# Kernel optimization log

Hardware: AMD Instinct MI355X
Metric: run time of the kernel (lower is better)

The kernel has to match this reference:

```python
import jax, jax.numpy as jnp
import numpy as np

B, N, E, D, F_IN, EDGE_DIM, VN = 128, 500, 1048576, 128, 5, 2, 10
NEG_FEAT = 0.01   # torch F.leaky_relu default
NEG_ATT = 0.2     # GAT attention slope


def _gat_layer(h_in, src, dst, edge_attr, W, b, a_src, a_dst, a_edge, We, n_nodes):
    # Edge-feature GAT conv: per-edge attention over (src, dst, edge) then
    # softmax-normalized scatter-aggregate onto destination nodes.
    h = h_in @ W                                  # [N, d]
    e = edge_attr @ We                            # [E, d] projected edge features
    logits = jax.nn.leaky_relu((h @ a_src)[src] + (h @ a_dst)[dst] + e @ a_edge,
                               negative_slope=NEG_ATT)    # [E]
    # segment softmax over incoming edges of each dst node
    m = jax.ops.segment_max(logits, dst, num_segments=n_nodes)
    ex = jnp.exp(logits - m[dst])
    denom = jax.ops.segment_sum(ex, dst, num_segments=n_nodes)
    alpha = ex / (denom[dst] + 1e-16)             # [E]
    msg = h[src] + e                              # [E, d]
    out = jax.ops.segment_sum(alpha[:, None] * msg, dst, num_segments=n_nodes)
    return out + b


def setup_inputs() -> dict:
    key = jax.random.key(0)
    ks = jax.random.split(key, 20)
    s = 0.05
    return {
        'x': jax.random.normal(ks[0], (B * N, F_IN), jnp.float32),
        'edge_index': jax.random.randint(ks[1], (2, E), 0, B * N, jnp.int64 if jax.config.jax_enable_x64 else jnp.int32).astype(jnp.int32),
        'edge_attr': jax.random.uniform(ks[2], (E, EDGE_DIM), jnp.float32),
        'curr_v_node_id': jax.random.randint(ks[3], (B,), 0, VN).astype(jnp.int32),
        'v_graph_embedding': jax.random.normal(ks[4], (B, D), jnp.float32),
        'v_node_dense_embeddings': jax.random.normal(ks[5], (B, VN, D), jnp.float32),
        'p_W': jax.random.normal(ks[6], (F_IN, D), jnp.float32) * s,
        'p_b': jnp.zeros((D,), jnp.float32),
        'Ws': jax.random.normal(ks[7], (4, D, D), jnp.float32) * s,
        'bs': jnp.zeros((4, D), jnp.float32),
        'a_srcs': jax.random.normal(ks[8], (4, D), jnp.float32) * s,
        'a_dsts': jax.random.normal(ks[9], (4, D), jnp.float32) * s,
        'a_edges': jax.random.normal(ks[10], (4, D), jnp.float32) * s,
        'Wes': jax.random.normal(ks[11], (4, EDGE_DIM, D), jnp.float32) * s,
        'W5': jax.random.normal(ks[12], (D, 1), jnp.float32) * s,
        'b5': jnp.zeros((1,), jnp.float32),
        'a_src5': jax.random.normal(ks[13], (1,), jnp.float32) * s,
        'a_dst5': jax.random.normal(ks[14], (1,), jnp.float32) * s,
        'a_edge5': jax.random.normal(ks[15], (1,), jnp.float32) * s,
        'We5': jax.random.normal(ks[16], (EDGE_DIM, 1), jnp.float32) * s,
    }


def reference(x, edge_index, edge_attr, curr_v_node_id, v_graph_embedding,
              v_node_dense_embeddings, p_W, p_b, Ws, bs, a_srcs, a_dsts,
              a_edges, Wes, W5, b5, a_src5, a_dst5, a_edge5, We5):
    n_nodes = x.shape[0]
    src, dst = edge_index[0], edge_index[1]
    # gather current v-node embedding: [B, D]
    curr_emb = v_node_dense_embeddings[jnp.arange(B), curr_v_node_id]
    # linear + leaky_relu then broadcast-add of graph/node context
    h = jax.nn.leaky_relu(x @ p_W + p_b, negative_slope=NEG_FEAT)  # [B*N, D]
    h = h.reshape(B, N, D) + v_graph_embedding[:, None, :] + curr_emb[:, None, :]
    h = h.reshape(B * N, D)
    # 4 hidden edge-feature GAT layers (128 -> 128) with leaky_relu
    for l in range(4):
        h = _gat_layer(h, src, dst, edge_attr, Ws[l], bs[l], a_srcs[l],
                       a_dsts[l], a_edges[l], Wes[l], n_nodes)
        h = jax.nn.leaky_relu(h, negative_slope=NEG_FEAT)
    # output layer (128 -> 1), no activation
    h = _gat_layer(h, src, dst, edge_attr, W5, b5, a_src5, a_dst5, a_edge5,
                   We5, n_nodes)                    # [B*N, 1]
    return h.reshape(B, N)
```

## Files before the change

### kernel.cpp

```cpp
#include <hip/hip_runtime.h>
#include <hip/hip_bf16.h>

#define BB   128
#define NN   500
#define NV   64000
#define EE   1048576
#define DD   128
#define FIN  5
#define VNN  10
#define NBUK 250
#define BCAP 8192

typedef unsigned int   uint32;
typedef unsigned short u16b;
typedef __attribute__((ext_vector_type(8))) short short8;
typedef __attribute__((ext_vector_type(4))) float float4v;
typedef __attribute__((ext_vector_type(2))) float float2v;

#define P_ASRC  0
#define P_ADST  512
#define P_WE    1024
#define P_BIAS  2048
#define P_W5    2560
#define P_CVEC  2688
#define P_SC5   2700
#define P_ASD   2816
#define P_TOT   3840

static __device__ __forceinline__ float bf2f(__hip_bfloat16 v) { return __bfloat162float(v); }
static __device__ __forceinline__ float lo2f(uint32 u) { return __uint_as_float(u << 16); }
static __device__ __forceinline__ float hi2f(uint32 u) { return __uint_as_float(u & 0xFFFF0000u); }
static __device__ __forceinline__ uint32 f2bf_bits(float f) {
    uint32 u = __float_as_uint(f);
    return (u + 0x7FFFu + ((u >> 16) & 1u)) >> 16;
}
static __device__ __forceinline__ uint32 pack2(float a, float b) {
    return (f2bf_bits(a) & 0xFFFFu) | (f2bf_bits(b) << 16);
}
static __device__ __forceinline__ float2v unp2(uint32 u) {
    float2v r; r.x = lo2f(u); r.y = hi2f(u); return r;
}
static __device__ __forceinline__ float2v fma2(float2v a, float2v b, float2v c) {
#if __has_builtin(__builtin_elementwise_fma)
    return __builtin_elementwise_fma(a, b, c);
#else
    float2v r; r.x = fmaf(a.x, b.x, c.x); r.y = fmaf(a.y, b.y, c.y); return r;
#endif
}
static __device__ __forceinline__ float2v fma2s(float2v a, float w, float2v c) {
    float2v ww = {w, w};
    return fma2(a, ww, c);
}
static __device__ __forceinline__ float2v shfl_xor2(float2v v, int o) {
    double d; __builtin_memcpy(&d, &v, 8);
    d = __shfl_xor(d, o, 64);
    float2v r; __builtin_memcpy(&r, &d, 8);
    return r;
}
static __device__ __forceinline__ float2v lrelu2(float2v x, float slope) {
    float2v z = {0.f, 0.f};
#if __has_builtin(__builtin_elementwise_max)
    float2v p = __builtin_elementwise_max(x, z);
    float2v q = __builtin_elementwise_min(x, z);
#else
    float2v p; p.x = fmaxf(x.x, 0.f); p.y = fmaxf(x.y, 0.f);
    float2v q; q.x = fminf(x.x, 0.f); q.y = fminf(x.y, 0.f);
#endif
    float2v s = {slope, slope};
    return fma2(q, s, p);
}
static __device__ __forceinline__ float ldf(const void* p, int i, int flag) {
    return flag ? ((const float*)p)[i] : bf2f(((const __hip_bfloat16*)p)[i]);
}

__global__ void sniff_init_kernel(const unsigned short* __restrict__ p16,
                                  int* __restrict__ FLAG, int* __restrict__ gcur,
                                  int* __restrict__ counts) {
    if (blockIdx.x == 0) {
        __shared__ int sHigh, sZero;
        if (threadIdx.x == 0) { sHigh = 0; sZero = 0; }
        __syncthreads();
        unsigned short v = p16[2 * threadIdx.x];
        if (v >= 0x8000u) atomicOr(&sHigh, 1);
        if (v == 0)       atomicAdd(&sZero, 1);
        __syncthreads();
        if (threadIdx.x == 0) FLAG[0] = (sHigh || sZero >= 128) ? 1 : 0;
    } else {
        int t = (blockIdx.x - 1) * 256 + threadIdx.x;
        if (t < NBUK) gcur[t] = t * BCAP;
        if (t < 512) counts[NV + t] = 0;
    }
}

__global__ void zero_out_kernel(void* __restrict__ out, const int* __restrict__ FLAG, float tag) {
    int i = blockIdx.x * blockDim.x + threadIdx.x;
    if (i >= NV) return;
    float v = (i == 0) ? tag : 0.f;
    if (FLAG[0]) ((float*)out)[i] = v;
    else         ((u16b*)out)[i] = (u16b)f2bf_bits(v);
}

__global__ __launch_bounds__(256) void prep_kernel(
        const void* __restrict__ Wes, const void* __restrict__ aeg,
        const void* __restrict__ We5, const void* __restrict__ ae5,
        const void* __restrict__ asr, const void* __restrict__ ads,
        const void* __restrict__ bs, const void* __restrict__ W5,
        const void* __restrict__ b5, const void* __restrict__ as5,
        const void* __restrict__ ad5, const void* __restrict__ Ws,
        const int* __restrict__ FLAG, float* __restrict__ PAR,
        u16b* __restrict__ WB) {
    const int flag = FLAG[0];
    if (blockIdx.x == 0) {
        for (int i = threadIdx.x; i < 512; i += 256) PAR[P_ASRC + i] = ldf(asr, i, flag);
    } else if (blockIdx.x == 1) {
        for (int i = threadIdx.x; i < 512; i += 256) PAR[P_ADST + i] = ldf(ads, i, flag);
    } else if (blockIdx.x == 2) {
        for (int i = threadIdx.x; i < 1024; i += 256) PAR[P_WE + i] = ldf(Wes, i, flag);
    } else if (blockIdx.x == 3) {
        for (int i = threadIdx.x; i < 512; i += 256) PAR[P_BIAS + i] = ldf(bs, i, flag);
    } else if (blockIdx.x == 4) {
        int tid = threadIdx.x;
        if (tid < 128) {
            PAR[P_W5 + tid] = ldf(W5, tid, flag);
        } else if (tid < 136) {
            int l = (tid - 128) >> 1, r = (tid - 128) & 1;
            float s = 0.f;
            for (int ch = 0; ch < DD; ++ch)
                s += ldf(Wes, l * 256 + r * DD + ch, flag) * ldf(aeg, l * DD + ch, flag);
            PAR[P_CVEC + l * 2 + r] = s;
        } else if (tid == 136) {
            float ae = ldf(ae5, 0, flag);
            float w0 = ldf(We5, 0, flag), w1 = ldf(We5, 1, flag);
            PAR[P_CVEC + 8] = w0 * ae; PAR[P_CVEC + 9] = w1 * ae;
            PAR[P_CVEC + 10] = w0;     PAR[P_CVEC + 11] = w1;
            PAR[P_SC5 + 0] = ldf(b5, 0, flag);
            PAR[P_SC5 + 1] = ldf(as5, 0, flag);
            PAR[P_SC5 + 2] = ldf(ad5, 0, flag);
        }
    } else if (blockIdx.x == 5) {
        for (int i = threadIdx.x; i < 512; i += 256) {
            int l = i >> 7, c = i & 127;
            PAR[P_ASD + l * 256 + c * 2]     = ldf(asr, l * DD + c, flag);
            PAR[P_ASD + l * 256 + c * 2 + 1] = ldf(ads, l * DD + c, flag);
        }
    } else {
        int t = (blockIdx.x - 6) * 256 + threadIdx.x;
        int lane = t & 63;
        int frag = t >> 6;
        int nchunk = frag & 7, kblk = (frag >> 3) & 3, l = frag >> 5;
        int n = nchunk * 16 + (lane & 15);
        int kbase = kblk * 32 + (lane >> 4) * 8;
#pragma unroll
        for (int j = 0; j < 8; ++j) {
            int idx = l * 16384 + (kbase + j) * 128 + n;
            u16b bits = flag ? (u16b)f2bf_bits(((const float*)Ws)[idx])
                             : ((const u16b*)Ws)[idx];
            WB[(size_t)t * 8 + j] = bits;
        }
    }
}

__global__ __launch_bounds__(256) void bucketize_kernel(
        const int* __restrict__ src, const int* __restrict__ dst,
        const void* __restrict__ eaP, const int* __restrict__ FLAG,
        int* __restrict__ gcur, uint32* __restrict__ bukx, uint32* __restrict__ buky) {
    __shared__ int cnt[256];
    __shared__ int cur[256];
    const int flag = FLAG[0];
    const int t = threadIdx.x;
    const int e0 = blockIdx.x * 4096;
    cnt[t] = 0;
    __syncthreads();
    int d[16];
#pragma unroll
    for (int i = 0; i < 16; ++i) {
        d[i] = dst[e0 + i * 256 + t];
        if ((unsigned)d[i] >= NV) d[i] = -1;
        if (d[i] >= 0) atomicAdd(&cnt[d[i] >> 8], 1);
    }
    __syncthreads();
    if (t < NBUK) {
        int c = cnt[t];
        cur[t] = c ? atomicAdd(&gcur[t], c) : 0;
    }
    __syncthreads();
#pragma unroll
    for (int i = 0; i < 16; ++i) {
        if (d[i] < 0) continue;
        int e = e0 + i * 256 + t;
        int b = d[i] >> 8;
        int s = src[e];
        if ((unsigned)s >= NV) s = 0;
        uint32 eb;
        if (flag) { float2 v = ((const float2*)eaP)[e]; eb = pack2(v.x, v.y); }
        else      eb = ((const uint32*)eaP)[e];
        int p = atomicAdd(&cur[b], 1);
        if (p < (b + 1) * BCAP) {
            bukx[p] = (uint32)((s & 0xFFFF) | ((d[i] & 255) << 16));
            buky[p] = eb;
        }
    }
}

__global__ __launch_bounds__(256) void bcount_kernel(
        const uint32* __restrict__ bukx, const int* __restrict__ gcur,
        int* __restrict__ counts) {
    __shared__ int c[256];
    const int b = blockIdx.x, t = threadIdx.x;
    c[t] = 0;
    __syncthreads();
    const int base = b * BCAP;
    int cnt = gcur[b] - base;
    if (cnt > BCAP) cnt = BCAP;
    for (int i = t; i < cnt; i += 256)
        atomicAdd(&c[(bukx[base + i] >> 16) & 255], 1);
    __syncthreads();
    counts[b * 256 + t] = c[t];
}

__global__ __launch_bounds__(256) void scan1_kernel(const int* __restrict__ counts,
                                                    int* __restrict__ row_ptr,
                                                    int* __restrict__ partials) {
    __shared__ int sdata[256];
    int tid = threadIdx.x;
    int4 v = ((const int4*)counts)[blockIdx.x * 256 + tid];
    int sum = v.x + v.y + v.z + v.w;
    sdata[tid] = sum;
    __syncthreads();
    int acc = sum;
    for (int off = 1; off < 256; off <<= 1) {
        int t = (tid >= off) ? sdata[tid - off] : 0;
        __syncthreads();
        acc += t;
        sdata[tid] = acc;
        __syncthreads();
    }
    int excl = acc - sum;
    int base = blockIdx.x * 1024 + tid * 4;
    int run = excl;
    if (base + 0 <= NV) row_ptr[base + 0] = run; run += v.x;
    if (base + 1 <= NV) row_ptr[base + 1] = run; run += v.y;
    if (base + 2 <= NV) row_ptr[base + 2] = run; run += v.z;
    if (base + 3 <= NV) row_ptr[base + 3] = run;
    if (tid == 255) partials[blockIdx.x] = acc;
}

__global__ __launch_bounds__(64) void scan2_kernel(const int* __restrict__ partials,
                                                   int* __restrict__ boff, int nb) {
    int lane = threadIdx.x;
    int v = (lane < nb) ? partials[lane] : 0;
    int orig = v;
#pragma unroll
    for (int off = 1; off < 64; off <<= 1) {
        int t = __shfl_up(v, off, 64);
        if (lane >= off) v += t;
    }
    boff[lane] = v - orig;
}

__global__ __launch_bounds__(256) void scan3_kernel(int* __restrict__ row_ptr,
                                                    const int* __restrict__ boff) {
    int add = boff[blockIdx.x];
    int base = blockIdx.x * 1024 + threadIdx.x * 4;
#pragma unroll
    for (int j = 0; j < 4; ++j) {
        int i = base + j;
        if (i <= NV) row_ptr[i] += add;
    }
}

__global__ __launch_bounds__(256) void bscatter_kernel(
        const uint32* __restrict__ bukx, const uint32* __restrict__ buky,
        const int* __restrict__ gcur, const int* __restrict__ row_ptr,
        uint2* __restrict__ csr2) {
    __shared__ int cur[256];
    const int b = blockIdx.x, t = threadIdx.x;
    cur[t] = row_ptr[b * 256 + t];
    __syncthreads();
    const int base = b * BCAP;
    int cnt = gcur[b] - base;
    if (cnt > BCAP) cnt = BCAP;
    for (int i = t; i < cnt; i += 256) {
        uint32 x = bukx[base + i];
        uint32 y = buky[base + i];
        int p = atomicAdd(&cur[(x >> 16) & 255], 1);
        csr2[p] = make_uint2(x & 0xFFFFu, y);
    }
}

__global__ __launch_bounds__(256) void gemm_kernel(
        const uint32* __restrict__ Hu, const u16b* __restrict__ WBl,
        const float* __restrict__ ASDl, uint32* __restrict__ HWu,
        float* __restrict__ ssrc, float* __restrict__ sdst) {
    __shared__ float hs[64 * 129];
    const int tid = threadIdx.x;
    const int lane = tid & 63;
    const int wave = tid >> 6;
    const int quad = lane >> 4;
    const int n0 = blockIdx.x * 64;
    const int m = n0 + wave * 16 + (lane & 15);

    const u16b* hrow = (const u16b*)Hu + (size_t)m * 128;
    short8 a0 = *(const short8*)(hrow + 0  + quad * 8);
    short8 a1 = *(const short8*)(hrow + 32 + quad * 8);
    short8 a2 = *(const short8*)(hrow + 64 + quad * 8);
    short8 a3 = *(const short8*)(hrow + 96 + quad * 8);

    const float2v* asd = (const float2v*)ASDl;
    float2v psd[4];
#pragma unroll
    for (int r = 0; r < 4; ++r) { psd[r].x = 0.f; psd[r].y = 0.f; }

#pragma unroll
    for (int nt = 0; nt < 8; ++nt) {
        const u16b* bbase = WBl + ((size_t)nt * 512 + lane * 8);
        short8 b0 = *(const short8*)(bbase + 0 * 4096);
        short8 b1 = *(const short8*)(bbase + 1 * 4096);
        short8 b2 = *(const short8*)(bbase + 2 * 4096);
        short8 b3 = *(const short8*)(bbase + 3 * 4096);
        float4v acc = {0.f, 0.f, 0.f, 0.f};
        acc = __builtin_amdgcn_mfma_f32_16x16x32_bf16(a0, b0, acc, 0, 0, 0);
        acc = __builtin_amdgcn_mfma_f32_16x16x32_bf16(a1, b1, acc, 0, 0, 0);
        acc = __builtin_amdgcn_mfma_f32_16x16x32_bf16(a2, b2, acc, 0, 0, 0);
        acc = __builtin_amdgcn_mfma_f32_16x16x32_bf16(a3, b3, acc, 0, 0, 0);
        float2v av = asd[nt * 16 + (lane & 15)];
#pragma unroll
        for (int r = 0; r < 4; ++r) {
            hs[(wave * 16 + quad * 4 + r) * 129 + nt * 16 + (lane & 15)] = acc[r];
            psd[r] = fma2s(av, acc[r], psd[r]);
        }
    }
#pragma unroll
    for (int r = 0; r < 4; ++r) {
#pragma unroll
        for (int o = 1; o < 16; o <<= 1) {
            float2v other = shfl_xor2(psd[r], o);
            psd[r].x += other.x; psd[r].y += other.y;
        }
    }
    if ((lane & 15) == 0) {
#pragma unroll
        for (int r = 0; r < 4; ++r) {
            int row = n0 + wave * 16 + quad * 4 + r;
            ssrc[row] = psd[r].x;
            sdst[row] = psd[r].y;
        }
    }
    __syncthreads();

#pragma unroll
    for (int i = 0; i < 4; ++i) {
        int flat = i * 2048 + tid * 8;
        int n = flat >> 7, c = flat & 127;
        const float* p = hs + n * 129 + c;
        uint4 v;
        v.x = pack2(p[0], p[1]); v.y = pack2(p[2], p[3]);
        v.z = pack2(p[4], p[5]); v.w = pack2(p[6], p[7]);
        *(uint4*)(HWu + (size_t)(n0 + n) * 64 + c / 2) = v;
    }
}

__global__ __launch_bounds__(256) void gemm_proj_kernel(
        const void* __restrict__ x, const void* __restrict__ pW,
        const void* __restrict__ pb, const int* __restrict__ curr,
        const void* __restrict__ vge, const void* __restrict__ vnd,
        const int* __restrict__ FLAG,
        const u16b* __restrict__ WBl, const float* __restrict__ ASDl,
        uint32* __restrict__ HWu, float* __restrict__ ssrc,
        float* __restrict__ sdst) {
    __shared__ float hs[64 * 129];
    uint32* Hl = (uint32*)hs;
    const int flag = FLAG[0];
    const int tid = threadIdx.x;
    const int lane = tid & 63;
    const int wave = tid >> 6;
    const int quad = lane >> 4;
    const int n0 = blockIdx.x * 64;

    {
        const int r = tid & 63;
        const int half = tid >> 6;
        const int n = n0 + r;
        const int b = n / NN;
        int cv = curr[b]; if ((unsigned)cv >= VNN) cv = 0;
        float xv[FIN];
#pragma unroll
        for (int k = 0; k < FIN; ++k) xv[k] = ldf(x, n * FIN + k, flag);
#pragma unroll
        for (int p = 0; p < 16; ++p) {
            const int c = half * 32 + p * 2;
            float s0 = ldf(pb, c, flag), s1 = ldf(pb, c + 1, flag);
#pragma unroll
            for (int k = 0; k < FIN; ++k) {
                s0 = fmaf(xv[k], ldf(pW, k * DD + c, flag), s0);
                s1 = fmaf(xv[k], ldf(pW, k * DD + c + 1, flag), s1);
            }
            s0 = (s0 > 0.f) ? s0 : 0.01f * s0;
            s1 = (s1 > 0.f) ? s1 : 0.01f * s1;
            s0 += ldf(vge, b * DD + c, flag) + ldf(vnd, (b * VNN + cv) * DD + c, flag);
            s1 += ldf(vge, b * DD + c + 1, flag) + ldf(vnd, (b * VNN + cv) * DD + c + 1, flag);
            Hl[r * 68 + half * 16 + p] = pack2(s0, s1);
        }
    }
    __syncthreads();

    const int mloc = wave * 16 + (lane & 15);
    short8 a0 = *(const short8*)(Hl + mloc * 68 + 0 * 16 + quad * 4);
    short8 a1 = *(const short8*)(Hl + mloc * 68 + 1 * 16 + quad * 4);
    short8 a2 = *(const short8*)(Hl + mloc * 68 + 2 * 16 + quad * 4);
    short8 a3 = *(const short8*)(Hl + mloc * 68 + 3 * 16 + quad * 4);
    __syncthreads();

    const float2v* asd = (const float2v*)ASDl;
    float2v psd[4];
#pragma unroll
    for (int r = 0; r < 4; ++r) { psd[r].x = 0.f; psd[r].y = 0.f; }

#pragma unroll
    for (int nt = 0; nt < 8; ++nt) {
        const u16b* bbase = WBl + ((size_t)nt * 512 + lane * 8);
        short8 b0 = *(const short8*)(bbase + 0 * 4096);
        short8 b1 = *(const short8*)(bbase + 1 * 4096);
        short8 b2 = *(const short8*)(bbase + 2 * 4096);
        short8 b3 = *(const short8*)(bbase + 3 * 4096);
        float4v acc = {0.f, 0.f, 0.f, 0.f};
        acc = __builtin_amdgcn_mfma_f32_16x16x32_bf16(a0, b0, acc, 0, 0, 0);
        acc = __builtin_amdgcn_mfma_f32_16x16x32_bf16(a1, b1, acc, 0, 0, 0);
        acc = __builtin_amdgcn_mfma_f32_16x16x32_bf16(a2, b2, acc, 0, 0, 0);
        acc = __builtin_amdgcn_mfma_f32_16x16x32_bf16(a3, b3, acc, 0, 0, 0);
        float2v av = asd[nt * 16 + (lane & 15)];
#pragma unroll
        for (int r = 0; r < 4; ++r) {
            hs[(wave * 16 + quad * 4 + r) * 129 + nt * 16 + (lane & 15)] = acc[r];
            psd[r] = fma2s(av, acc[r], psd[r]);
        }
    }
#pragma unroll
    for (int r = 0; r < 4; ++r) {
#pragma unroll
        for (int o = 1; o < 16; o <<= 1) {
            float2v other = shfl_xor2(psd[r], o);
            psd[r].x += other.x; psd[r].y += other.y;
        }
    }
    if ((lane & 15) == 0) {
#pragma unroll
        for (int r = 0; r < 4; ++r) {
            int row = n0 + wave * 16 + quad * 4 + r;
            ssrc[row] = psd[r].x;
            sdst[row] = psd[r].y;
        }
    }
    __syncthreads();

#pragma unroll
    for (int i = 0; i < 4; ++i) {
        int flat = i * 2048 + tid * 8;
        int n = flat >> 7, c = flat & 127;
        const float* p = hs + n * 129 + c;
        uint4 v;
        v.x = pack2(p[0], p[1]); v.y = pack2(p[2], p[3]);
        v.z = pack2(p[4], p[5]); v.w = pack2(p[6], p[7]);
        *(uint4*)(HWu + (size_t)(n0 + n) * 64 + c / 2) = v;
    }
}

__global__ __launch_bounds__(256) void agg_kernel(
        const uint32* __restrict__ HWu, const float* __restrict__ ssrc,
        const float* __restrict__ sdst, const uint2* __restrict__ csr2,
        const int* __restrict__ row_ptr, const float* __restrict__ PAR,
        int layer, uint32* __restrict__ HoutU,
        float* __restrict__ hw5out, int wantw5) {
    __shared__ float exs[4][64];
    const int lane = threadIdx.x & 63;
    const int wid = threadIdx.x >> 6;
    const int n = blockIdx.x * 4 + wid;
    const int begin = __builtin_amdgcn_readfirstlane(row_ptr[n]);
    const int deg   = __builtin_amdgcn_readfirstlane(row_ptr[n + 1]) - begin;
    const float c0 = PAR[P_CVEC + 2 * layer], c1 = PAR[P_CVEC + 2 * layer + 1];
    const float sd = sdst[n];

    int   sv = 0;
    uint32 eb = 0;
    if (lane < deg) {
        uint2 se = csr2[begin + lane];
        sv = (int)se.x;
        eb = se.y;
    }
    const float ssv = ssrc[sv];

    const int dmain = (deg < 64) ? deg : 64;
    const int npad  = (dmain + 15) & ~15;

    uint32 hA[16], hB[16];
#pragma unroll
    for (int q = 0; q < 16; ++q) {
        int s = __builtin_amdgcn_readlane(sv, q);
        hA[q] = HWu[(s << 6) + lane];
    }
    if (npad > 16) {
#pragma unroll
        for (int q = 0; q < 16; ++q) {
            int s = __builtin_amdgcn_readlane(sv, 16 + q);
            hB[q] = HWu[(s << 6) + lane];
        }
    }

    float ex = 0.f;
    if (lane < deg) {
        float L = fmaf(hi2f(eb), c1, fmaf(lo2f(eb), c0, ssv + sd));
        L = (L > 0.f) ? L : 0.2f * L;
        ex = __expf(fminf(L, 60.f));
    }
    exs[wid][lane] = ex;

    float2v acc2 = {0.f, 0.f};
    const float* wp = &exs[wid][0];
#pragma unroll
    for (int q0 = 0; q0 < 16; q0 += 4) {
        float4 w4 = *(const float4*)(wp + q0);
        acc2 = fma2s(unp2(hA[q0 + 0]), w4.x, acc2);
        acc2 = fma2s(unp2(hA[q0 + 1]), w4.y, acc2);
        acc2 = fma2s(unp2(hA[q0 + 2]), w4.z, acc2);
        acc2 = fma2s(unp2(hA[q0 + 3]), w4.w, acc2);
    }
    if (npad > 16) {
#pragma unroll
        for (int q0 = 16; q0 < 32; q0 += 4) {
            float4 w4 = *(const float4*)(wp + q0);
            acc2 = fma2s(unp2(hB[q0 - 16]), w4.x, acc2);
            acc2 = fma2s(unp2(hB[q0 - 15]), w4.y, acc2);
            acc2 = fma2s(unp2(hB[q0 - 14]), w4.z, acc2);
            acc2 = fma2s(unp2(hB[q0 - 13]), w4.w, acc2);
        }
    }
    for (int j = 32; j < dmain; ++j) {
        int s = __builtin_amdgcn_readlane(sv, j);
        float w = wp[j];
        acc2 = fma2s(unp2(HWu[(s << 6) + lane]), w, acc2);
    }

    float dsum = ex;
    float2v sxy = unp2(eb);
    sxy.x *= ex; sxy.y *= ex;
    for (int j0 = 64; j0 < deg; j0 += 64) {
        int j = j0 + lane;
        if (j < deg) {
            uint2 se2 = csr2[begin + j];
            float L2 = fmaf(hi2f(se2.y), c1, fmaf(lo2f(se2.y), c0, ssrc[se2.x] + sd));
            L2 = (L2 > 0.f) ? L2 : 0.2f * L2;
            float x2 = __expf(fminf(L2, 60.f));
            dsum += x2;
            sxy = fma2s(unp2(se2.y), x2, sxy);
        }
    }
#pragma unroll
    for (int o = 32; o; o >>= 1) {
        dsum += __shfl_xor(dsum, o, 64);
        float2v other = shfl_xor2(sxy, o);
        sxy.x += other.x; sxy.y += other.y;
    }

    for (int jj = 64; jj < deg; ++jj) {
        uint2 se2 = csr2[begin + jj];
        float L2 = fmaf(hi2f(se2.y), c1, fmaf(lo2f(se2.y), c0, ssrc[se2.x] + sd));
        L2 = (L2 > 0.f) ? L2 : 0.2f * L2;
        float x2 = __expf(fminf(L2, 60.f));
        acc2 = fma2s(unp2(HWu[(size_t)se2.x * 64 + lane]), x2, acc2);
    }

    const int ch = lane * 2;
    const float* WEl = PAR + P_WE + layer * 256;
    const float inv = __builtin_amdgcn_rcpf(dsum + 1e-16f);
    const float* Bl = PAR + P_BIAS + layer * DD;
    float2v we0 = *(const float2v*)(WEl + ch);
    float2v we1 = *(const float2v*)(WEl + DD + ch);
    float2v bl  = *(const float2v*)(Bl + ch);
    float2v t2 = fma2s(we1, sxy.y, fma2s(we0, sxy.x, acc2));
    float2v o2 = fma2s(t2, inv, bl);
    o2 = lrelu2(o2, 0.01f);

    if (!wantw5) {
        HoutU[(size_t)n * 64 + lane] = pack2(o2.x, o2.y);
    } else {
        float p = o2.x * PAR[P_W5 + ch] + o2.y * PAR[P_W5 + ch + 1];
#pragma unroll
        for (int o = 32; o; o >>= 1) p += __shfl_xor(p, o, 64);
        if (lane == 0) hw5out[n] = p;
    }
}

__global__ __launch_bounds__(256) void final_kernel(
        const float* __restrict__ hw5, const uint2* __restrict__ csr2,
        const int* __restrict__ row_ptr, const float* __restrict__ PAR,
        const int* __restrict__ FLAG, void* __restrict__ out) {
    const int flag = FLAG[0];
    int lane = threadIdx.x & 63;
    int n = blockIdx.x * 4 + (threadIdx.x >> 6);
    int begin = __builtin_amdgcn_readfirstlane(row_ptr[n]);
    int deg   = __builtin_amdgcn_readfirstlane(row_ptr[n + 1]) - begin;
    float c50 = PAR[P_CVEC + 8], c51 = PAR[P_CVEC + 9];
    float ce0 = PAR[P_CVEC + 10], ce1 = PAR[P_CVEC + 11];
    float b5v = PAR[P_SC5], a5s = PAR[P_SC5 + 1];
    float hd = PAR[P_SC5 + 2] * hw5[n];

    float dsum = 0.f, msum = 0.f;
    for (int j0 = 0; j0 < deg; j0 += 64) {
        int j = j0 + lane;
        if (j < deg) {
            uint2 se = csr2[begin + j];
            float hs5 = hw5[se.x];
            float L = fmaf(hi2f(se.y), c51, fmaf(lo2f(se.y), c50, fmaf(a5s, hs5, hd)));
            L = (L > 0.f) ? L : 0.2f * L;
            float ex = __expf(fminf(L, 60.f));
            dsum += ex;
            msum = fmaf(ex, hs5 + fmaf(hi2f(se.y), ce1, lo2f(se.y) * ce0), msum);
        }
    }
#pragma unroll
    for (int o = 32; o; o >>= 1) {
        dsum += __shfl_xor(dsum, o, 64);
        msum += __shfl_xor(msum, o, 64);
    }
    if (lane == 0) {
        float r = msum * __builtin_amdgcn_rcpf(dsum + 1e-16f) + b5v;
        if (flag) ((float*)out)[n] = r;
        else      ((u16b*)out)[n] = (u16b)f2bf_bits(r);
    }
}

extern "C" void kernel_launch(void* const* d_in, const int* in_sizes, int n_in,
                              void* d_out, int out_size, void* d_ws, size_t ws_size,
                              hipStream_t stream) {
    const void* x   = d_in[0];
    const int*  ei  = (const int*)d_in[1];
    const void* ea  = d_in[2];
    const int*  cur = (const int*)d_in[3];
    const void* vge = d_in[4];
    const void* vnd = d_in[5];
    const void* pW  = d_in[6];
    const void* pb  = d_in[7];
    const void* Ws  = d_in[8];
    const void* bs  = d_in[9];
    const void* asr = d_in[10];
    const void* ads = d_in[11];
    const void* aeg = d_in[12];
    const void* Wes = d_in[13];
    const void* W5  = d_in[14];
    const void* b5  = d_in[15];
    const void* as5 = d_in[16];
    const void* ad5 = d_in[17];
    const void* ae5 = d_in[18];
    const void* We5 = d_in[19];
    (void)in_sizes; (void)n_in; (void)out_size;

    const int* e_src = ei;
    const int* e_dst = ei + EE;

    size_t off = 0;
    char* base = (char*)d_ws;
    auto carve = [&](size_t bytes) {
        void* p = base + off;
        off += (bytes + 255) & ~(size_t)255;
        return p;
    };
    int*    FLAG   = (int*)carve(256);
    float*  PAR    = (float*)carve((size_t)P_TOT * 4);
    u16b*   WB     = (u16b*)carve(4 * DD * DD * 2);
    uint32* H0     = (uint32*)carve((size_t)NV * DD * 2);
    uint32* H1     = (uint32*)carve((size_t)NV * DD * 2);
    float*  SS     = (float*)carve(NV * 4);
    float*  SD     = (float*)carve(NV * 4);
    float*  HW5v   = (float*)carve(NV * 4);
    int*    COUNTS = (int*)carve(65536 * 4);
    int*    ROWPTR = (int*)carve(65536 * 4);
    int*    GCUR   = (int*)carve(256 * 4);
    int*    PART   = (int*)carve(256 * 4);
    int*    BOFF   = (int*)carve(256 * 4);
    uint2*  CSR2   = (uint2*)carve((size_t)EE * 8);
    size_t need = off;

    uint32* BUKX = H1;
    uint32* BUKY = H1 + (size_t)NBUK * BCAP;

    sniff_init_kernel<<<3, 256, 0, stream>>>((const unsigned short*)ea, FLAG,
                                             GCUR, COUNTS);

    if (need > ws_size) {
        zero_out_kernel<<<(NV + 255) / 256, 256, 0, stream>>>(
            d_out, FLAG, (float)(ws_size >> 20));
        return;
    }

    prep_kernel<<<38, 256, 0, stream>>>(Wes, aeg, We5, ae5, asr, ads, bs,
                                        W5, b5, as5, ad5, Ws, FLAG, PAR, WB);

    bucketize_kernel<<<EE / 4096, 256, 0, stream>>>(e_src, e_dst, ea, FLAG,
                                                    GCUR, BUKX, BUKY);
    bcount_kernel<<<NBUK, 256, 0, stream>>>(BUKX, GCUR, COUNTS);
    scan1_kernel<<<63, 256, 0, stream>>>(COUNTS, ROWPTR, PART);
    scan2_kernel<<<1, 64, 0, stream>>>(PART, BOFF, 63);
    scan3_kernel<<<63, 256, 0, stream>>>(ROWPTR, BOFF);
    bscatter_kernel<<<NBUK, 256, 0, stream>>>(BUKX, BUKY, GCUR, ROWPTR, CSR2);

    gemm_proj_kernel<<<NV / 64, 256, 0, stream>>>(
        x, pW, pb, cur, vge, vnd, FLAG, WB, PAR + P_ASD, H1, SS, SD);
    agg_kernel<<<NV / 4, 256, 0, stream>>>(
        H1, SS, SD, CSR2, ROWPTR, PAR, 0, H0, HW5v, 0);
    for (int l = 1; l < 4; ++l) {
        gemm_kernel<<<NV / 64, 256, 0, stream>>>(
            H0, WB + (size_t)l * 16384, PAR + P_ASD + l * 256, H1, SS, SD);
        agg_kernel<<<NV / 4, 256, 0, stream>>>(
            H1, SS, SD, CSR2, ROWPTR, PAR, l, H0, HW5v, (l == 3) ? 1 : 0);
    }

    final_kernel<<<NV / 4, 256, 0, stream>>>(HW5v, CSR2, ROWPTR, PAR,
                                             FLAG, d_out);
}
```

Before: 385.5 us.

## Fuse prep with bucketize, count degrees via global atomics, pack GEMM epilogue in bf16

Merges the weight-prep and edge-bucketize kernels into one launch and removes the separate bucket-count pass by incrementing global per-node counters with atomics during bucketization. A small init kernel zeroes those counters. The GEMM epilogues now pack bf16 pairs via lane shuffles into a smaller shared tile instead of staging full fp32 rows. The aggregation kernel loads neighbor rows in chunks of 8 gated by degree, to avoid wasted gathers for low-degree nodes. The trade-off is about a million global atomics on the counters in exchange for one fewer kernel and pass over the buckets.

```diff
diff --git a/kernel.cpp b/kernel.cpp
--- a/kernel.cpp
+++ b/kernel.cpp
@@ -73,23 +73,15 @@
     return flag ? ((const float*)p)[i] : bf2f(((const __hip_bfloat16*)p)[i]);
 }
 
-__global__ void sniff_init_kernel(const unsigned short* __restrict__ p16,
-                                  int* __restrict__ FLAG, int* __restrict__ gcur,
-                                  int* __restrict__ counts) {
-    if (blockIdx.x == 0) {
-        __shared__ int sHigh, sZero;
-        if (threadIdx.x == 0) { sHigh = 0; sZero = 0; }
-        __syncthreads();
-        unsigned short v = p16[2 * threadIdx.x];
-        if (v >= 0x8000u) atomicOr(&sHigh, 1);
-        if (v == 0)       atomicAdd(&sZero, 1);
-        __syncthreads();
-        if (threadIdx.x == 0) FLAG[0] = (sHigh || sZero >= 128) ? 1 : 0;
-    } else {
-        int t = (blockIdx.x - 1) * 256 + threadIdx.x;
-        if (t < NBUK) gcur[t] = t * BCAP;
-        if (t < 512) counts[NV + t] = 0;
-    }
+__global__ void sniff_kernel(const unsigned short* __restrict__ p16, int* __restrict__ FLAG) {
+    __shared__ int sHigh, sZero;
+    if (threadIdx.x == 0) { sHigh = 0; sZero = 0; }
+    __syncthreads();
+    unsigned short v = p16[2 * threadIdx.x];
+    if (v >= 0x8000u) atomicOr(&sHigh, 1);
+    if (v == 0)       atomicAdd(&sZero, 1);
+    __syncthreads();
+    if (threadIdx.x == 0) FLAG[0] = (sHigh || sZero >= 128) ? 1 : 0;
 }
 
 __global__ void zero_out_kernel(void* __restrict__ out, const int* __restrict__ FLAG, float tag) {
@@ -100,15 +92,25 @@
     else         ((u16b*)out)[i] = (u16b)f2bf_bits(v);
 }
 
-__global__ __launch_bounds__(256) void prep_kernel(
+__global__ void init_kernel(int* __restrict__ gcur, int* __restrict__ counts) {
+    int i = blockIdx.x * 1024 + threadIdx.x * 4;
+    if (i < NV + 512) *(int4*)(counts + i) = make_int4(0, 0, 0, 0);
+    int t = blockIdx.x * 256 + threadIdx.x;
+    if (t < NBUK) gcur[t] = t * BCAP;
+}
+
+__global__ __launch_bounds__(256) void prep_bucketize_kernel(
         const void* __restrict__ Wes, const void* __restrict__ aeg,
         const void* __restrict__ We5, const void* __restrict__ ae5,
         const void* __restrict__ asr, const void* __restrict__ ads,
         const void* __restrict__ bs, const void* __restrict__ W5,
         const void* __restrict__ b5, const void* __restrict__ as5,
         const void* __restrict__ ad5, const void* __restrict__ Ws,
-        const int* __restrict__ FLAG, float* __restrict__ PAR,
-        u16b* __restrict__ WB) {
+        const int* __restrict__ src, const int* __restrict__ dst,
+        const void* __restrict__ eaP, const int* __restrict__ FLAG,
+        float* __restrict__ PAR, u16b* __restrict__ WB,
+        int* __restrict__ gcur, uint32* __restrict__ bukx,
+        uint32* __restrict__ buky, int* __restrict__ counts) {
     const int flag = FLAG[0];
     if (blockIdx.x == 0) {
         for (int i = threadIdx.x; i < 512; i += 256) PAR[P_ASRC + i] = ldf(asr, i, flag);
@@ -143,7 +145,7 @@
             PAR[P_ASD + l * 256 + c * 2]     = ldf(asr, l * DD + c, flag);
             PAR[P_ASD + l * 256 + c * 2 + 1] = ldf(ads, l * DD + c, flag);
         }
-    } else {
+    } else if (blockIdx.x < 38) {
         int t = (blockIdx.x - 6) * 256 + threadIdx.x;
         int lane = t & 63;
         int frag = t >> 6;
@@ -157,65 +159,44 @@
                              : ((const u16b*)Ws)[idx];
             WB[(size_t)t * 8 + j] = bits;
         }
-    }
-}
-
-__global__ __launch_bounds__(256) void bucketize_kernel(
-        const int* __restrict__ src, const int* __restrict__ dst,
-        const void* __restrict__ eaP, const int* __restrict__ FLAG,
-        int* __restrict__ gcur, uint32* __restrict__ bukx, uint32* __restrict__ buky) {
-    __shared__ int cnt[256];
-    __shared__ int cur[256];
-    const int flag = FLAG[0];
-    const int t = threadIdx.x;
-    const int e0 = blockIdx.x * 4096;
-    cnt[t] = 0;
-    __syncthreads();
-    int d[16];
-#pragma unroll
-    for (int i = 0; i < 16; ++i) {
-        d[i] = dst[e0 + i * 256 + t];
-        if ((unsigned)d[i] >= NV) d[i] = -1;
-        if (d[i] >= 0) atomicAdd(&cnt[d[i] >> 8], 1);
-    }
-    __syncthreads();
-    if (t < NBUK) {
-        int c = cnt[t];
-        cur[t] = c ? atomicAdd(&gcur[t], c) : 0;
-    }
-    __syncthreads();
-#pragma unroll
-    for (int i = 0; i < 16; ++i) {
-        if (d[i] < 0) continue;
-        int e = e0 + i * 256 + t;
-        int b = d[i] >> 8;
-        int s = src[e];
-        if ((unsigned)s >= NV) s = 0;
-        uint32 eb;
-        if (flag) { float2 v = ((const float2*)eaP)[e]; eb = pack2(v.x, v.y); }
-        else      eb = ((const uint32*)eaP)[e];
-        int p = atomicAdd(&cur[b], 1);
-        if (p < (b + 1) * BCAP) {
-            bukx[p] = (uint32)((s & 0xFFFF) | ((d[i] & 255) << 16));
-            buky[p] = eb;
-        }
-    }
-}
-
-__global__ __launch_bounds__(256) void bcount_kernel(
-        const uint32* __restrict__ bukx, const int* __restrict__ gcur,
-        int* __restrict__ counts) {
-    __shared__ int c[256];
-    const int b = blockIdx.x, t = threadIdx.x;
-    c[t] = 0;
-    __syncthreads();
-    const int base = b * BCAP;
-    int cnt = gcur[b] - base;
-    if (cnt > BCAP) cnt = BCAP;
-    for (int i = t; i < cnt; i += 256)
-        atomicAdd(&c[(bukx[base + i] >> 16) & 255], 1);
-    __syncthreads();
-    counts[b * 256 + t] = c[t];
+    } else {
+        __shared__ int cnt[256];
+        __shared__ int cur[256];
+        const int t = threadIdx.x;
+        const int e0 = (blockIdx.x - 38) * 4096;
+        cnt[t] = 0;
+        __syncthreads();
+        int d[16];
+#pragma unroll
+        for (int i = 0; i < 16; ++i) {
+            d[i] = dst[e0 + i * 256 + t];
+            if ((unsigned)d[i] >= NV) d[i] = -1;
+            if (d[i] >= 0) atomicAdd(&cnt[d[i] >> 8], 1);
+        }
+        __syncthreads();
+        if (t < NBUK) {
+            int c = cnt[t];
+            cur[t] = c ? atomicAdd(&gcur[t], c) : 0;
+        }
+        __syncthreads();
+#pragma unroll
+        for (int i = 0; i < 16; ++i) {
+            if (d[i] < 0) continue;
+            int e = e0 + i * 256 + t;
+            int bk = d[i] >> 8;
+            int s = src[e];
+            if ((unsigned)s >= NV) s = 0;
+            uint32 eb;
+            if (flag) { float2 v = ((const float2*)eaP)[e]; eb = pack2(v.x, v.y); }
+            else      eb = ((const uint32*)eaP)[e];
+            int p = atomicAdd(&cur[bk], 1);
+            if (p < (bk + 1) * BCAP) {
+                bukx[p] = (uint32)((s & 0xFFFF) | ((d[i] & 255) << 16));
+                buky[p] = eb;
+                atomicAdd(&counts[d[i]], 1);
+            }
+        }
+    }
 }
 
 __global__ __launch_bounds__(256) void scan1_kernel(const int* __restrict__ counts,
@@ -292,7 +273,7 @@
         const uint32* __restrict__ Hu, const u16b* __restrict__ WBl,
         const float* __restrict__ ASDl, uint32* __restrict__ HWu,
         float* __restrict__ ssrc, float* __restrict__ sdst) {
-    __shared__ float hs[64 * 129];
+    __shared__ uint32 cs[64 * 68];
     const int tid = threadIdx.x;
     const int lane = tid & 63;
     const int wave = tid >> 6;
@@ -326,8 +307,12 @@
         float2v av = asd[nt * 16 + (lane & 15)];
 #pragma unroll
         for (int r = 0; r < 4; ++r) {
-            hs[(wave * 16 + quad * 4 + r) * 129 + nt * 16 + (lane & 15)] = acc[r];
             psd[r] = fma2s(av, acc[r], psd[r]);
+            float vn = __shfl_xor(acc[r], 1, 64);
+            if (!(lane & 1)) {
+                int row = wave * 16 + quad * 4 + r;
+                cs[row * 68 + nt * 8 + ((lane & 15) >> 1)] = pack2(acc[r], vn);
+            }
         }
     }
 #pragma unroll
@@ -349,14 +334,11 @@
     __syncthreads();
 
 #pragma unroll
-    for (int i = 0; i < 4; ++i) {
-        int flat = i * 2048 + tid * 8;
-        int n = flat >> 7, c = flat & 127;
-        const float* p = hs + n * 129 + c;
-        uint4 v;
-        v.x = pack2(p[0], p[1]); v.y = pack2(p[2], p[3]);
-        v.z = pack2(p[4], p[5]); v.w = pack2(p[6], p[7]);
-        *(uint4*)(HWu + (size_t)(n0 + n) * 64 + c / 2) = v;
+    for (int j = 0; j < 4; ++j) {
+        int idx = j * 256 + tid;
+        int row = idx >> 4, w = (idx & 15) * 4;
+        uint4 v = *(const uint4*)(cs + row * 68 + w);
+        *(uint4*)(HWu + (size_t)(n0 + row) * 64 + w) = v;
     }
 }
 
@@ -368,8 +350,7 @@
         const u16b* __restrict__ WBl, const float* __restrict__ ASDl,
         uint32* __restrict__ HWu, float* __restrict__ ssrc,
         float* __restrict__ sdst) {
-    __shared__ float hs[64 * 129];
-    uint32* Hl = (uint32*)hs;
+    __shared__ uint32 cs[64 * 68];
     const int flag = FLAG[0];
     const int tid = threadIdx.x;
     const int lane = tid & 63;
@@ -399,16 +380,16 @@
             s1 = (s1 > 0.f) ? s1 : 0.01f * s1;
             s0 += ldf(vge, b * DD + c, flag) + ldf(vnd, (b * VNN + cv) * DD + c, flag);
             s1 += ldf(vge, b * DD + c + 1, flag) + ldf(vnd, (b * VNN + cv) * DD + c + 1, flag);
-            Hl[r * 68 + half * 16 + p] = pack2(s0, s1);
+            cs[r * 68 + half * 16 + p] = pack2(s0, s1);
         }
     }
     __syncthreads();
 
     const int mloc = wave * 16 + (lane & 15);
-    short8 a0 = *(const short8*)(Hl + mloc * 68 + 0 * 16 + quad * 4);
-    short8 a1 = *(const short8*)(Hl + mloc * 68 + 1 * 16 + quad * 4);
-    short8 a2 = *(const short8*)(Hl + mloc * 68 + 2 * 16 + quad * 4);
-    short8 a3 = *(const short8*)(Hl + mloc * 68 + 3 * 16 + quad * 4);
+    short8 a0 = *(const short8*)(cs + mloc * 68 + 0 * 16 + quad * 4);
+    short8 a1 = *(const short8*)(cs + mloc * 68 + 1 * 16 + quad * 4);
+    short8 a2 = *(const short8*)(cs + mloc * 68 + 2 * 16 + quad * 4);
+    short8 a3 = *(const short8*)(cs + mloc * 68 + 3 * 16 + quad * 4);
     __syncthreads();
 
     const float2v* asd = (const float2v*)ASDl;
@@ -431,8 +412,12 @@
         float2v av = asd[nt * 16 + (lane & 15)];
 #pragma unroll
         for (int r = 0; r < 4; ++r) {
-            hs[(wave * 16 + quad * 4 + r) * 129 + nt * 16 + (lane & 15)] = acc[r];
             psd[r] = fma2s(av, acc[r], psd[r]);
+            float vn = __shfl_xor(acc[r], 1, 64);
+            if (!(lane & 1)) {
+                int row = wave * 16 + quad * 4 + r;
+                cs[row * 68 + nt * 8 + ((lane & 15) >> 1)] = pack2(acc[r], vn);
+            }
         }
     }
 #pragma unroll
@@ -454,14 +439,11 @@
     __syncthreads();
 
 #pragma unroll
-    for (int i = 0; i < 4; ++i) {
-        int flat = i * 2048 + tid * 8;
-        int n = flat >> 7, c = flat & 127;
-        const float* p = hs + n * 129 + c;
-        uint4 v;
-        v.x = pack2(p[0], p[1]); v.y = pack2(p[2], p[3]);
-        v.z = pack2(p[4], p[5]); v.w = pack2(p[6], p[7]);
-        *(uint4*)(HWu + (size_t)(n0 + n) * 64 + c / 2) = v;
+    for (int j = 0; j < 4; ++j) {
+        int idx = j * 256 + tid;
+        int row = idx >> 4, w = (idx & 15) * 4;
+        uint4 v = *(const uint4*)(cs + row * 68 + w);
+        *(uint4*)(HWu + (size_t)(n0 + row) * 64 + w) = v;
     }
 }
 
@@ -490,19 +472,34 @@
     const float ssv = ssrc[sv];
 
     const int dmain = (deg < 64) ? deg : 64;
-    const int npad  = (dmain + 15) & ~15;
-
-    uint32 hA[16], hB[16];
-#pragma unroll
-    for (int q = 0; q < 16; ++q) {
-        int s = __builtin_amdgcn_readlane(sv, q);
-        hA[q] = HWu[(s << 6) + lane];
-    }
-    if (npad > 16) {
-#pragma unroll
-        for (int q = 0; q < 16; ++q) {
+
+    uint32 h0[8], h1[8], h2[8], h3[8];
+    if (dmain > 0) {
+#pragma unroll
+        for (int q = 0; q < 8; ++q) {
+            int s = __builtin_amdgcn_readlane(sv, q);
+            h0[q] = HWu[(s << 6) + lane];
+        }
+    }
+    if (dmain > 8) {
+#pragma unroll
+        for (int q = 0; q < 8; ++q) {
+            int s = __builtin_amdgcn_readlane(sv, 8 + q);
+            h1[q] = HWu[(s << 6) + lane];
+        }
+    }
+    if (dmain > 16) {
+#pragma unroll
+        for (int q = 0; q < 8; ++q) {
             int s = __builtin_amdgcn_readlane(sv, 16 + q);
-            hB[q] = HWu[(s << 6) + lane];
+            h2[q] = HWu[(s << 6) + lane];
+        }
+    }
+    if (dmain > 24) {
+#pragma unroll
+        for (int q = 0; q < 8; ++q) {
+            int s = __builtin_amdgcn_readlane(sv, 24 + q);
+            h3[q] = HWu[(s << 6) + lane];
         }
     }
 
@@ -516,22 +513,44 @@
 
     float2v acc2 = {0.f, 0.f};
     const float* wp = &exs[wid][0];
-#pragma unroll
-    for (int q0 = 0; q0 < 16; q0 += 4) {
-        float4 w4 = *(const float4*)(wp + q0);
-        acc2 = fma2s(unp2(hA[q0 + 0]), w4.x, acc2);
-        acc2 = fma2s(unp2(hA[q0 + 1]), w4.y, acc2);
-        acc2 = fma2s(unp2(hA[q0 + 2]), w4.z, acc2);
-        acc2 = fma2s(unp2(hA[q0 + 3]), w4.w, acc2);
-    }
-    if (npad > 16) {
-#pragma unroll
-        for (int q0 = 16; q0 < 32; q0 += 4) {
+    if (dmain > 0) {
+#pragma unroll
+        for (int q0 = 0; q0 < 8; q0 += 4) {
             float4 w4 = *(const float4*)(wp + q0);
-            acc2 = fma2s(unp2(hB[q0 - 16]), w4.x, acc2);
-            acc2 = fma2s(unp2(hB[q0 - 15]), w4.y, acc2);
-            acc2 = fma2s(unp2(hB[q0 - 14]), w4.z, acc2);
-            acc2 = fma2s(unp2(hB[q0 - 13]), w4.w, acc2);
+            acc2 = fma2s(unp2(h0[q0 + 0]), w4.x, acc2);
+            acc2 = fma2s(unp2(h0[q0 + 1]), w4.y, acc2);
+            acc2 = fma2s(unp2(h0[q0 + 2]), w4.z, acc2);
+            acc2 = fma2s(unp2(h0[q0 + 3]), w4.w, acc2);
+        }
+    }
+    if (dmain > 8) {
+#pragma unroll
+        for (int q0 = 8; q0 < 16; q0 += 4) {
+            float4 w4 = *(const float4*)(wp + q0);
+            acc2 = fma2s(unp2(h1[q0 - 8]), w4.x, acc2);
+            acc2 = fma2s(unp2(h1[q0 - 7]), w4.y, acc2);
+            acc2 = fma2s(unp2(h1[q0 - 6]), w4.z, acc2);
+            acc2 = fma2s(unp2(h1[q0 - 5]), w4.w, acc2);
+        }
+    }
+    if (dmain > 16) {
+#pragma unroll
+        for (int q0 = 16; q0 < 24; q0 += 4) {
+            float4 w4 = *(const float4*)(wp + q0);
+            acc2 = fma2s(unp2(h2[q0 - 16]), w4.x, acc2);
+            acc2 = fma2s(unp2(h2[q0 - 15]), w4.y, acc2);
+            acc2 = fma2s(unp2(h2[q0 - 14]), w4.z, acc2);
+            acc2 = fma2s(unp2(h2[q0 - 13]), w4.w, acc2);
+        }
+    }
+    if (dmain > 24) {
+#pragma unroll
+        for (int q0 = 24; q0 < 32; q0 += 4) {
+            float4 w4 = *(const float4*)(wp + q0);
+            acc2 = fma2s(unp2(h3[q0 - 24]), w4.x, acc2);
+            acc2 = fma2s(unp2(h3[q0 - 23]), w4.y, acc2);
+            acc2 = fma2s(unp2(h3[q0 - 22]), w4.z, acc2);
+            acc2 = fma2s(unp2(h3[q0 - 21]), w4.w, acc2);
         }
     }
     for (int j = 32; j < dmain; ++j) {
@@ -683,8 +702,7 @@
     uint32* BUKX = H1;
     uint32* BUKY = H1 + (size_t)NBUK * BCAP;
 
-    sniff_init_kernel<<<3, 256, 0, stream>>>((const unsigned short*)ea, FLAG,
-                                             GCUR, COUNTS);
+    sniff_kernel<<<1, 256, 0, stream>>>((const unsigned short*)ea, FLAG);
 
     if (need > ws_size) {
         zero_out_kernel<<<(NV + 255) / 256, 256, 0, stream>>>(
@@ -692,12 +710,10 @@
         return;
     }
 
-    prep_kernel<<<38, 256, 0, stream>>>(Wes, aeg, We5, ae5, asr, ads, bs,
-                                        W5, b5, as5, ad5, Ws, FLAG, PAR, WB);
-
-    bucketize_kernel<<<EE / 4096, 256, 0, stream>>>(e_src, e_dst, ea, FLAG,
-                                                    GCUR, BUKX, BUKY);
-    bcount_kernel<<<NBUK, 256, 0, stream>>>(BUKX, GCUR, COUNTS);
+    init_kernel<<<64, 256, 0, stream>>>(GCUR, COUNTS);
+    prep_bucketize_kernel<<<294, 256, 0, stream>>>(
+        Wes, aeg, We5, ae5, asr, ads, bs, W5, b5, as5, ad5, Ws,
+        e_src, e_dst, ea, FLAG, PAR, WB, GCUR, BUKX, BUKY, COUNTS);
     scan1_kernel<<<63, 256, 0, stream>>>(COUNTS, ROWPTR, PART);
     scan2_kernel<<<1, 64, 0, stream>>>(PART, BOFF, 63);
     scan3_kernel<<<63, 256, 0, stream>>>(ROWPTR, BOFF);
```

Result: slower. 411.1 us (+6.6%).
